# Kernel tuning notes

Measured on AMD Instinct MI355X. Metric: run time of the kernel, lower is better.

Reference implementation:

```python
import jax, jax.numpy as jnp
import numpy as np

B, T, D_IN = 64, 365, 10
D_MODEL, N_HEAD, D_K = 256, 16, 8
D_HEAD = D_MODEL // N_HEAD  # 16, value head dim
MAX_POS = 365 + 2 * 30      # max_position + 2*max_temporal_shift = 425
BN_EPS = 1e-5


def _pos_table(n_pos, d, temp=1000.0):
    # standard sinusoidal table (frozen in the original via Embedding.from_pretrained)
    pos = np.arange(n_pos)[:, None].astype(np.float64)
    i = np.arange(d)[None, :]
    angle = pos / np.power(temp, 2 * (i // 2) / d)
    tab = np.where(i % 2 == 0, np.sin(angle), np.cos(angle))
    return jnp.asarray(tab, jnp.float32)

POS_TABLE = _pos_table(MAX_POS, D_MODEL)


def _linear_layer(x, W, b, g, beta):
    # LinearLayer = Linear -> BatchNorm1d (train-mode batch stats, per-feature) -> ReLU
    y = x @ W.T + b
    ax = tuple(range(y.ndim - 1))
    mu = y.mean(ax, keepdims=True)
    var = y.var(ax, keepdims=True)  # biased var, matches torch BN
    y = (y - mu) * jax.lax.rsqrt(var + BN_EPS) * g + beta
    return jax.nn.relu(y)


def _forward(positions, x, w1, b1, g1, e1, w2, b2, g2, e2, w3, b3, g3, e3,
             ws1, ws2, wi, bi, gi, ei, wk, bk, wq, bq, wm, bm, gm, em,
             wd1, bd1, gd1, ed1, wd2, bd2, gd2, ed2, wc, bc):
    # channel MLP encoder: 10 -> 64 -> 128 -> 256
    out = _linear_layer(x, w1, b1, g1, e1)
    out = _linear_layer(out, w2, b2, g2, e2)
    out = _linear_layer(out, w3, b3, g3, e3)                    # [B,T,256]
    # channel SE attention: avgpool over time, 2 linears (no bias), sigmoid, residual
    pooled = out.mean(axis=1, keepdims=True)                     # [B,1,256]
    att = jax.nn.sigmoid(jax.nn.relu(pooled @ ws1.T) @ ws2.T)    # [B,1,256]
    out = att * pooled + out                                     # broadcast residual
    # temporal attention block
    h = _linear_layer(out, wi, bi, gi, ei)                       # inconv -> [B,T,256]
    e = h + POS_TABLE[positions]                                 # add positional encoding
    q = (e @ wq.T + bq).reshape(B, T, N_HEAD, D_K)
    k = (e @ wk.T + bk).reshape(B, T, N_HEAD, D_K)
    v = e.reshape(B, T, N_HEAD, D_HEAD)
    # 'cross' attention: full score matrix, mean over key dim, softmax over query dim
    scores = jnp.einsum('bthd,bshd->bhts', q, k) / jnp.sqrt(jnp.float32(D_K))  # [B,H,T,T]
    scores = scores.mean(axis=-1)                                # [B,H,T]
    a = jax.nn.softmax(scores, axis=-1)                          # [B,H,T]
    y = jnp.einsum('bht,bthe->bhe', a, v).reshape(B, D_MODEL)    # [B,256]
    y = _linear_layer(y, wm, bm, gm, em)                         # mlp 256 -> 128
    # decoder: 128 -> 64 -> 32 -> num_classes
    z = _linear_layer(y, wd1, bd1, gd1, ed1)
    z = _linear_layer(z, wd2, bd2, gd2, ed2)
    return z @ wc.T + bc                                         # logits [B,10]


def setup_inputs():
    key = jax.random.key(0)
    ks = jax.random.split(key, 16)
    n = lambda i, sh: jax.random.normal(ks[i], sh, jnp.float32) * 0.05
    z, o = jnp.zeros, jnp.ones
    return {
        'x': jax.random.normal(ks[0], (B, T, D_IN), jnp.float32),
        'positions': jnp.sort(jax.random.randint(ks[1], (B, T), 0, MAX_POS), axis=-1),
        'w1': n(2, (64, D_IN)), 'b1': z(64), 'g1': o(64), 'e1': z(64),
        'w2': n(3, (128, 64)), 'b2': z(128), 'g2': o(128), 'e2': z(128),
        'w3': n(4, (256, 128)), 'b3': z(256), 'g3': o(256), 'e3': z(256),
        'ws1': n(5, (16, 256)), 'ws2': n(6, (256, 16)),
        'wi': n(7, (256, 256)), 'bi': z(256), 'gi': o(256), 'ei': z(256),
        'wk': n(8, (128, 256)), 'bk': z(128),
        'wq': n(9, (128, 256)), 'bq': z(128),
        'wm': n(10, (128, 256)), 'bm': z(128), 'gm': o(128), 'em': z(128),
        'wd1': n(11, (64, 128)), 'bd1': z(64), 'gd1': o(64), 'ed1': z(64),
        'wd2': n(12, (32, 64)), 'bd2': z(32), 'gd2': o(32), 'ed2': z(32),
        'wc': n(13, (10, 32)), 'bc': z(10),
    }


def reference(x, positions, w1, b1, g1, e1, w2, b2, g2, e2, w3, b3, g3, e3,
              ws1, ws2, wi, bi, gi, ei, wk, bk, wq, bq, wm, bm, gm, em,
              wd1, bd1, gd1, ed1, wd2, bd2, gd2, ed2, wc, bc):
    return _forward(positions, x, w1, b1, g1, e1, w2, b2, g2, e2, w3, b3, g3, e3,
                    ws1, ws2, wi, bi, gi, ei, wk, bk, wq, bq, wm, bm, gm, em,
                    wd1, bd1, gd1, ed1, wd2, bd2, gd2, ed2, wc, bc)
```

## Files before the change

kernel.cpp:

```cpp
#include <hip/hip_runtime.h>
#include <hip/hip_bf16.h>
#include <math.h>

#define TT 365
#define BT 23360
#define NPOS 425

typedef __hip_bfloat16 bf16;
typedef __attribute__((ext_vector_type(8))) short s16x8;
typedef __attribute__((ext_vector_type(4))) float f32x4;

__device__ __forceinline__ float b2f(bf16 v) { return __bfloat162float(v); }
__device__ __forceinline__ bf16  f2b(float v) { return __float2bfloat16(v); }
__device__ __forceinline__ float u2f(unsigned u) { return __uint_as_float(u); }
__device__ __forceinline__ short f2bs(float v) { bf16 h = __float2bfloat16(v); return *reinterpret_cast<short*>(&h); }
__device__ __forceinline__ void unpack8(uint4 raw, float* v) {
    v[0] = u2f(raw.x << 16); v[1] = u2f(raw.x & 0xffff0000u);
    v[2] = u2f(raw.y << 16); v[3] = u2f(raw.y & 0xffff0000u);
    v[4] = u2f(raw.z << 16); v[5] = u2f(raw.z & 0xffff0000u);
    v[6] = u2f(raw.w << 16); v[7] = u2f(raw.w & 0xffff0000u);
}

__global__ __launch_bounds__(256) void prep_kernel(
    float* __restrict__ stats, float* __restrict__ pooled, float* __restrict__ esum,
    const float* __restrict__ w2, const float* __restrict__ w3, const float* __restrict__ wi,
    const float* __restrict__ wq,
    bf16* __restrict__ whi, bf16* __restrict__ wlo, float* __restrict__ tab)
{
    int i = blockIdx.x * 256 + threadIdx.x;
    if (i < 2048)  { stats[i] = 0.f; return; }  i -= 2048;
    if (i < 16384) { pooled[i] = 0.f; return; } i -= 16384;
    if (i < 16384) { esum[i] = 0.f; return; }   i -= 16384;
    if (i < 139264) {
        float w;
        if      (i < 8192)   w = w2[i];
        else if (i < 40960)  w = w3[i - 8192];
        else if (i < 106496) w = wi[i - 40960];
        else                 w = wq[i - 106496];
        bf16 h = f2b(w);
        whi[i] = h;
        wlo[i] = f2b(w - b2f(h));
        return;
    } i -= 139264;
    if (i < 108800) {
        int c = i & 255, p = i >> 8;
        float e = (float)(2 * (c >> 1)) * (1.f / 256.f);
        float ang = (float)p * exp2f(-e * 9.96578428466209f);
        tab[i] = (c & 1) ? cosf(ang) : sinf(ang);
    }
}

__global__ __launch_bounds__(256) void gemm_l1_kernel(
    const float* __restrict__ x,
    const float* __restrict__ W, const float* __restrict__ bias,
    bf16* __restrict__ Y, float* __restrict__ stats)
{
    const int t  = threadIdx.x;
    const int tx = t & 15, ty = t >> 4;
    const int row0 = blockIdx.x * 64;
    __shared__ float As[64][17];
    __shared__ float Ws[16][65];
    __shared__ float red_s[4][64];
    __shared__ float red_q[4][64];
    float acc[4][4];
#pragma unroll
    for (int rr = 0; rr < 4; ++rr)
#pragma unroll
        for (int cc = 0; cc < 4; ++cc) acc[rr][cc] = 0.f;
#pragma unroll
    for (int i = 0; i < 4; ++i) {
        int idx = t + i * 256, r = idx >> 4, c = idx & 15;
        As[r][c] = (c < 10) ? x[(size_t)(row0 + r) * 10 + c] : 0.f;
    }
#pragma unroll
    for (int i = 0; i < 4; ++i) {
        int idx = t + i * 256, c = idx >> 4, kk = idx & 15;
        Ws[kk][c] = (kk < 10) ? W[(size_t)c * 10 + kk] : 0.f;
    }
    __syncthreads();
#pragma unroll
    for (int kk = 0; kk < 10; ++kk) {
        float a[4];
#pragma unroll
        for (int rr = 0; rr < 4; ++rr) a[rr] = As[ty * 4 + rr][kk];
#pragma unroll
        for (int cc = 0; cc < 4; ++cc) {
            float w = Ws[kk][cc * 16 + tx];
#pragma unroll
            for (int rr = 0; rr < 4; ++rr) acc[rr][cc] = fmaf(a[rr], w, acc[rr][cc]);
        }
    }
    float s_cc[4], q_cc[4];
#pragma unroll
    for (int cc = 0; cc < 4; ++cc) { s_cc[cc] = 0.f; q_cc[cc] = 0.f; }
#pragma unroll
    for (int rr = 0; rr < 4; ++rr) {
        int row = row0 + ty * 4 + rr;
#pragma unroll
        for (int cc = 0; cc < 4; ++cc) {
            int col = cc * 16 + tx;
            float v = acc[rr][cc] + bias[col];
            Y[(size_t)row * 64 + col] = f2b(v);
            s_cc[cc] += v; q_cc[cc] += v * v;
        }
    }
    int w = t >> 6;
#pragma unroll
    for (int cc = 0; cc < 4; ++cc) {
        float s = s_cc[cc], q = q_cc[cc];
        s += __shfl_xor(s, 16); q += __shfl_xor(q, 16);
        s += __shfl_xor(s, 32); q += __shfl_xor(q, 32);
        if ((t & 63) < 16) { red_s[w][cc * 16 + tx] = s; red_q[w][cc * 16 + tx] = q; }
    }
    __syncthreads();
    if (t < 64) {
        float s = red_s[0][t] + red_s[1][t] + red_s[2][t] + red_s[3][t];
        float q = red_q[0][t] + red_q[1][t] + red_q[2][t] + red_q[3][t];
        atomicAdd(&stats[t], s);
        atomicAdd(&stats[256 + t], q);
    }
}

template<int MODE, int K>
__global__ __launch_bounds__(256) void mfma_gemm(
    const bf16* __restrict__ A,
    const bf16* __restrict__ Whi, const bf16* __restrict__ Wlo,
    const float* __restrict__ bias,
    bf16* __restrict__ Y, int ldY, float* __restrict__ stats,
    const float* __restrict__ bnstats, const float* __restrict__ bng,
    const float* __restrict__ bnb, const float* __restrict__ sebuf)
{
    constexpr int KC = (K > 128) ? 128 : K;
    __shared__ s16x8 Wl[2][KC / 8][64];
    __shared__ float red_s[4][64];
    __shared__ float red_q[4][64];
    __shared__ float scb[MODE ? K : 1];
    __shared__ float shb[MODE ? K : 1];
    const int t = threadIdx.x, wave = t >> 6, lane = t & 63;
    const int n16 = lane & 15, quad = lane >> 4;
    const int m0 = blockIdx.x * 64 + wave * 16;
    const int col0 = blockIdx.y * 64;
    const int sc_ = t & 63, skg0 = t >> 6;
    const bf16* gh = Whi + (size_t)(col0 + sc_) * K;
    const bf16* gl = Wlo + (size_t)(col0 + sc_) * K;
#pragma unroll
    for (int kg = skg0; kg < KC / 8; kg += 4) {
        Wl[0][kg][sc_] = *(const s16x8*)(gh + kg * 8);
        Wl[1][kg][sc_] = *(const s16x8*)(gl + kg * 8);
    }
    if (MODE) {
        if (t < K) {
            float mu = bnstats[t] * (1.f / (float)BT);
            float var = bnstats[256 + t] * (1.f / (float)BT) - mu * mu;
            float sc = rsqrtf(var + 1e-5f) * bng[t];
            scb[t] = sc; shb[t] = bnb[t] - mu * sc;
        }
    }
    __syncthreads();
    const int arow = m0 + n16;
    const float* sev = (MODE == 2) ? (sebuf + (arow / TT) * 256) : nullptr;
    const bf16* Ap = A + (size_t)arow * K + quad * 8;
    s16x8 af[K / 32];
#pragma unroll
    for (int i = 0; i < K / 32; ++i) {
        s16x8 raw = *(const s16x8*)(Ap + i * 32);
        if (MODE) {
            int kb = i * 32 + quad * 8;
#pragma unroll
            for (int j = 0; j < 8; ++j) {
                float y = u2f(((unsigned)(unsigned short)raw[j]) << 16);
                float v = fmaxf(fmaf(y, scb[kb + j], shb[kb + j]), 0.f);
                if (MODE == 2) v += sev[kb + j];
                raw[j] = f2bs(v);
            }
        }
        af[i] = raw;
    }
    f32x4 acc[4];
    f32x4 zero = {0.f, 0.f, 0.f, 0.f};
#pragma unroll
    for (int ct = 0; ct < 4; ++ct) acc[ct] = zero;
#pragma unroll
    for (int kc = 0; kc < K; kc += KC) {
        if (kc) {
            __syncthreads();
#pragma unroll
            for (int kg = skg0; kg < KC / 8; kg += 4) {
                Wl[0][kg][sc_] = *(const s16x8*)(gh + kc + kg * 8);
                Wl[1][kg][sc_] = *(const s16x8*)(gl + kc + kg * 8);
            }
            __syncthreads();
        }
#pragma unroll
        for (int i = 0; i < KC / 32; ++i) {
            const int kgq = i * 4 + quad;
            const s16x8 a = af[(kc >> 5) + i];
#pragma unroll
            for (int ct = 0; ct < 4; ++ct) {
                s16x8 bl = Wl[1][kgq][ct * 16 + n16];
                s16x8 bh = Wl[0][kgq][ct * 16 + n16];
                acc[ct] = __builtin_amdgcn_mfma_f32_16x16x32_bf16(a, bl, acc[ct], 0, 0, 0);
                acc[ct] = __builtin_amdgcn_mfma_f32_16x16x32_bf16(a, bh, acc[ct], 0, 0, 0);
            }
        }
    }
#pragma unroll
    for (int ct = 0; ct < 4; ++ct) {
        int col = col0 + ct * 16 + n16;
        float bv = bias[col];
        float s = 0.f, q = 0.f;
#pragma unroll
        for (int r = 0; r < 4; ++r) {
            float v = acc[ct][r] + bv;
            int row = m0 + quad * 4 + r;
            Y[(size_t)row * ldY + col] = f2b(v);
            s += v; q += v * v;
        }
        s += __shfl_xor(s, 16); q += __shfl_xor(q, 16);
        s += __shfl_xor(s, 32); q += __shfl_xor(q, 32);
        if (quad == 0) { red_s[wave][ct * 16 + n16] = s; red_q[wave][ct * 16 + n16] = q; }
    }
    if (stats) {
        __syncthreads();
        if (t < 64) {
            float s = red_s[0][t] + red_s[1][t] + red_s[2][t] + red_s[3][t];
            float q = red_q[0][t] + red_q[1][t] + red_q[2][t] + red_q[3][t];
            atomicAdd(&stats[col0 + t], s);
            atomicAdd(&stats[256 + col0 + t], q);
        }
    }
}

__global__ __launch_bounds__(256) void pool_partial_kernel(
    const bf16* __restrict__ Y3, const float* __restrict__ stats,
    const float* __restrict__ g3, const float* __restrict__ e3,
    float* __restrict__ pooled)
{
    const int b = blockIdx.x, part = blockIdx.y, t = threadIdx.x;
    const int cg = t & 31, rs = t >> 5;
    __shared__ float scb[256], shb[256];
    __shared__ float pp[8][256];
    {
        float mu = stats[t] * (1.f / (float)BT);
        float var = stats[256 + t] * (1.f / (float)BT) - mu * mu;
        float sc = rsqrtf(var + 1e-5f) * g3[t];
        scb[t] = sc; shb[t] = e3[t] - mu * sc;
    }
    __syncthreads();
    float acc[8] = {0.f,0.f,0.f,0.f,0.f,0.f,0.f,0.f};
    const int r0 = part * 46;
#pragma unroll
    for (int i = 0; i < 6; ++i) {
        int l = rs + i * 8;
        int r = r0 + l;
        if (l < 46 && r < TT) {
            uint4 raw = *(const uint4*)(Y3 + ((size_t)b * TT + r) * 256 + cg * 8);
            float v[8];
            unpack8(raw, v);
#pragma unroll
            for (int j = 0; j < 8; ++j)
                acc[j] += fmaxf(fmaf(v[j], scb[cg * 8 + j], shb[cg * 8 + j]), 0.f);
        }
    }
#pragma unroll
    for (int j = 0; j < 8; ++j) pp[rs][cg * 8 + j] = acc[j];
    __syncthreads();
    float s = 0.f;
#pragma unroll
    for (int r = 0; r < 8; ++r) s += pp[r][t];
    atomicAdd(&pooled[b * 256 + t], s);
}

__global__ __launch_bounds__(256) void esum_kernel(const bf16* __restrict__ e,
                                                   float* __restrict__ esum)
{
    const int b = blockIdx.x, part = blockIdx.y, t = threadIdx.x;
    const int cg = t & 31, rs = t >> 5;
    __shared__ float pp[8][256];
    float acc[8] = {0.f,0.f,0.f,0.f,0.f,0.f,0.f,0.f};
    const int r0 = part * 46;
#pragma unroll
    for (int i = 0; i < 6; ++i) {
        int l = rs + i * 8;
        int r = r0 + l;
        if (l < 46 && r < TT) {
            uint4 raw = *(const uint4*)(e + ((size_t)b * TT + r) * 256 + cg * 8);
            float v[8];
            unpack8(raw, v);
#pragma unroll
            for (int j = 0; j < 8; ++j) acc[j] += v[j];
        }
    }
#pragma unroll
    for (int j = 0; j < 8; ++j) pp[rs][cg * 8 + j] = acc[j];
    __syncthreads();
    float s = 0.f;
#pragma unroll
    for (int r = 0; r < 8; ++r) s += pp[r][t];
    atomicAdd(&esum[b * 256 + t], s);
}

__global__ __launch_bounds__(256) void se_mlp_kernel(const float* __restrict__ pooled,
                                                     const float* __restrict__ ws1,
                                                     const float* __restrict__ ws2,
                                                     float* __restrict__ se) {
    int b = blockIdx.x, f = threadIdx.x;
    __shared__ float pl[256];
    __shared__ float hidden[16];
    float p = pooled[b * 256 + f] * (1.f / (float)TT);
    pl[f] = p;
    __syncthreads();
    if (f < 16) {
        float h = 0.f;
        for (int k2 = 0; k2 < 256; ++k2) h = fmaf(pl[k2], ws1[f * 256 + k2], h);
        hidden[f] = fmaxf(h, 0.f);
    }
    __syncthreads();
    float a = 0.f;
    for (int k2 = 0; k2 < 16; ++k2) a = fmaf(hidden[k2], ws2[f * 16 + k2], a);
    a = 1.f / (1.f + expf(-a));
    se[b * 256 + f] = a * p;
}

__global__ __launch_bounds__(256) void bnrelu8_kernel(
    const bf16* __restrict__ Y, const float* __restrict__ stats,
    const float* __restrict__ g, const float* __restrict__ beta,
    bf16* __restrict__ Out, const float* __restrict__ tab, const int* __restrict__ pos) {
    int i = (blockIdx.x * 256 + threadIdx.x) * 8;
    int col = i & 255, row = i >> 8;
    uint4 raw = *(const uint4*)(Y + i);
    float v[8];
    unpack8(raw, v);
    const float invM = 1.f / (float)BT;
    const float* tr = tab + pos[row] * 256 + col;
    bf16 tmp[8] __attribute__((aligned(16)));
#pragma unroll
    for (int j = 0; j < 8; ++j) {
        float mu  = stats[col + j] * invM;
        float var = stats[256 + col + j] * invM - mu * mu;
        float o = (v[j] - mu) * rsqrtf(var + 1e-5f) * g[col + j] + beta[col + j];
        tmp[j] = f2b(fmaxf(o, 0.f) + tr[j]);
    }
    *(uint4*)(Out + i) = *(const uint4*)tmp;
}

__global__ __launch_bounds__(64) void attn_kernel(
    const bf16* __restrict__ q, const bf16* __restrict__ e,
    const float* __restrict__ esum, const float* __restrict__ wk,
    const float* __restrict__ bk, float* __restrict__ yv)
{
    __shared__ float aw[368];
    const int b = blockIdx.x, h = blockIdx.y;
    const int lane = threadIdx.x;
    float4 es = *(const float4*)(esum + b * 256 + lane * 4);
    float ks[8];
#pragma unroll
    for (int d = 0; d < 8; ++d) {
        float4 wv = *(const float4*)(wk + (size_t)(h * 8 + d) * 256 + lane * 4);
        ks[d] = es.x * wv.x + es.y * wv.y + es.z * wv.z + es.w * wv.w;
    }
#pragma unroll
    for (int off = 1; off < 64; off <<= 1)
#pragma unroll
        for (int d = 0; d < 8; ++d) ks[d] += __shfl_xor(ks[d], off);
#pragma unroll
    for (int d = 0; d < 8; ++d) ks[d] += (float)TT * bk[h * 8 + d];
    const float scale = 1.f / (sqrtf(8.f) * (float)TT);
    const bf16* qb = q + (size_t)b * TT * 128 + h * 8;
    float sv[6];
    float m = -1e30f;
#pragma unroll
    for (int i = 0; i < 6; ++i) {
        int r = lane + i * 64;
        float s = -1e30f;
        if (r < TT) {
            uint4 raw = *(const uint4*)(qb + (size_t)r * 128);
            float v[8];
            unpack8(raw, v);
            float dot = 0.f;
#pragma unroll
            for (int j = 0; j < 8; ++j) dot = fmaf(v[j], ks[j], dot);
            s = dot * scale;
        }
        sv[i] = s;
        m = fmaxf(m, s);
    }
#pragma unroll
    for (int off = 1; off < 64; off <<= 1) m = fmaxf(m, __shfl_xor(m, off));
    float sum = 0.f;
#pragma unroll
    for (int i = 0; i < 6; ++i) {
        float ev = (sv[i] > -1e29f) ? expf(sv[i] - m) : 0.f;
        sv[i] = ev; sum += ev;
    }
#pragma unroll
    for (int off = 1; off < 64; off <<= 1) sum += __shfl_xor(sum, off);
    float inv = 1.f / sum;
#pragma unroll
    for (int i = 0; i < 6; ++i) {
        int r = lane + i * 64;
        if (r < TT) aw[r] = sv[i] * inv;
    }
    __syncthreads();
    const int half = lane & 1, rs = lane >> 1;
    float acc[8] = {0.f,0.f,0.f,0.f,0.f,0.f,0.f,0.f};
    const bf16* ebase = e + (size_t)b * TT * 256 + h * 16 + half * 8;
#pragma unroll
    for (int i = 0; i < 12; ++i) {
        int r = rs + i * 32;
        if (r < TT) {
            uint4 raw = *(const uint4*)(ebase + (size_t)r * 256);
            float v[8];
            unpack8(raw, v);
            float a = aw[r];
#pragma unroll
            for (int j = 0; j < 8; ++j) acc[j] = fmaf(a, v[j], acc[j]);
        }
    }
#pragma unroll
    for (int off = 2; off < 64; off <<= 1)
#pragma unroll
        for (int j = 0; j < 8; ++j) acc[j] += __shfl_xor(acc[j], off);
    if (lane < 2) {
        float* op = yv + b * 256 + h * 16 + half * 8;
#pragma unroll
        for (int j = 0; j < 8; ++j) op[j] = acc[j];
    }
}


__global__ __launch_bounds__(256) void tail_m_kernel(
    const float* __restrict__ yv, const float* __restrict__ wm,
    const float* __restrict__ gm, const float* __restrict__ em,
    float* __restrict__ z1)
{
    __shared__ float Xq[4160];
    const int t = threadIdx.x, r = t & 63, cw = t >> 6;
    const int c0 = blockIdx.x * 8 + cw * 2;
    const float4* wf4 = (const float4*)wm;
    float acc[2] = {0.f, 0.f};
    for (int p = 0; p < 4; ++p) {
        if (p) __syncthreads();
        for (int i = t; i < 4096; i += 256) {
            int kk = i & 63, rr = i >> 6;
            Xq[kk * 65 + rr] = yv[rr * 256 + p * 64 + kk];
        }
        __syncthreads();
#pragma unroll 4
        for (int k4 = 0; k4 < 16; ++k4) {
            float xv[4];
#pragma unroll
            for (int j = 0; j < 4; ++j) xv[j] = Xq[(k4 * 4 + j) * 65 + r];
#pragma unroll
            for (int c = 0; c < 2; ++c) {
                float4 w = wf4[(c0 + c) * 64 + p * 16 + k4];
                acc[c] = fmaf(xv[0], w.x, acc[c]);
                acc[c] = fmaf(xv[1], w.y, acc[c]);
                acc[c] = fmaf(xv[2], w.z, acc[c]);
                acc[c] = fmaf(xv[3], w.w, acc[c]);
            }
        }
    }
#pragma unroll
    for (int c = 0; c < 2; ++c) {
        float v = acc[c];
        float s = v, q = v * v;
#pragma unroll
        for (int off = 1; off < 64; off <<= 1) { s += __shfl_xor(s, off); q += __shfl_xor(q, off); }
        float mu = s * (1.f / 64.f), var = q * (1.f / 64.f) - mu * mu;
        float sc = rsqrtf(var + 1e-5f) * gm[c0 + c], sh = em[c0 + c] - mu * sc;
        z1[r * 128 + c0 + c] = fmaxf(fmaf(v, sc, sh), 0.f);
    }
}

__global__ __launch_bounds__(256) void tail_d1_kernel(
    const float* __restrict__ z1, const float* __restrict__ wd1,
    const float* __restrict__ gd1, const float* __restrict__ ed1,
    float* __restrict__ z2)
{
    __shared__ float Xq[4160];
    const int t = threadIdx.x, r = t & 63, cw = t >> 6;
    const int c0 = blockIdx.x * 8 + cw * 2;
    const float4* wf4 = (const float4*)wd1;
    float acc[2] = {0.f, 0.f};
    for (int p = 0; p < 2; ++p) {
        if (p) __syncthreads();
        for (int i = t; i < 4096; i += 256) {
            int kk = i & 63, rr = i >> 6;
            Xq[kk * 65 + rr] = z1[rr * 128 + p * 64 + kk];
        }
        __syncthreads();
#pragma unroll 4
        for (int k4 = 0; k4 < 16; ++k4) {
            float xv[4];
#pragma unroll
            for (int j = 0; j < 4; ++j) xv[j] = Xq[(k4 * 4 + j) * 65 + r];
#pragma unroll
            for (int c = 0; c < 2; ++c) {
                float4 w = wf4[(c0 + c) * 32 + p * 16 + k4];
                acc[c] = fmaf(xv[0], w.x, acc[c]);
                acc[c] = fmaf(xv[1], w.y, acc[c]);
                acc[c] = fmaf(xv[2], w.z, acc[c]);
                acc[c] = fmaf(xv[3], w.w, acc[c]);
            }
        }
    }
#pragma unroll
    for (int c = 0; c < 2; ++c) {
        float v = acc[c];
        float s = v, q = v * v;
#pragma unroll
        for (int off = 1; off < 64; off <<= 1) { s += __shfl_xor(s, off); q += __shfl_xor(q, off); }
        float mu = s * (1.f / 64.f), var = q * (1.f / 64.f) - mu * mu;
        float sc = rsqrtf(var + 1e-5f) * gd1[c0 + c], sh = ed1[c0 + c] - mu * sc;
        z2[r * 64 + c0 + c] = fmaxf(fmaf(v, sc, sh), 0.f);
    }
}

__global__ __launch_bounds__(256) void tail_d2c_kernel(
    const float* __restrict__ z2, const float* __restrict__ wd2,
    const float* __restrict__ gd2, const float* __restrict__ ed2,
    const float* __restrict__ wc, const float* __restrict__ bc,
    float* __restrict__ out)
{
    __shared__ float Xq[4160];
    __shared__ float Z3t[2048];
    __shared__ float WcL[320];
    const int t = threadIdx.x, r = t & 63, cw = t >> 6;
    const int c03 = cw * 8;
    for (int i = t; i < 4096; i += 256) {
        int kk = i & 63, rr = i >> 6;
        Xq[kk * 65 + rr] = z2[rr * 64 + kk];
    }
    if (t < 80) ((float4*)WcL)[t] = ((const float4*)wc)[t];
    __syncthreads();
    const float4* wf4 = (const float4*)wd2;
    float acc[8] = {0.f,0.f,0.f,0.f,0.f,0.f,0.f,0.f};
#pragma unroll 4
    for (int k4 = 0; k4 < 16; ++k4) {
        float xv[4];
#pragma unroll
        for (int j = 0; j < 4; ++j) xv[j] = Xq[(k4 * 4 + j) * 65 + r];
#pragma unroll
        for (int c = 0; c < 8; ++c) {
            float4 w = wf4[(c03 + c) * 16 + k4];
            acc[c] = fmaf(xv[0], w.x, acc[c]);
            acc[c] = fmaf(xv[1], w.y, acc[c]);
            acc[c] = fmaf(xv[2], w.z, acc[c]);
            acc[c] = fmaf(xv[3], w.w, acc[c]);
        }
    }
#pragma unroll
    for (int c = 0; c < 8; ++c) {
        float v = acc[c];
        float s = v, q = v * v;
#pragma unroll
        for (int off = 1; off < 64; off <<= 1) { s += __shfl_xor(s, off); q += __shfl_xor(q, off); }
        float mu = s * (1.f / 64.f), var = q * (1.f / 64.f) - mu * mu;
        float sc = rsqrtf(var + 1e-5f) * gd2[c03 + c], sh = ed2[c03 + c] - mu * sc;
        Z3t[(c03 + c) * 64 + r] = fmaxf(fmaf(v, sc, sh), 0.f);
    }
    __syncthreads();
#pragma unroll
    for (int i = 0; i < 3; ++i) {
        int idx = t + i * 256;
        if (idx < 640) {
            int rr = idx / 10, c = idx - rr * 10;
            float s = bc[c];
#pragma unroll
            for (int kk = 0; kk < 32; ++kk) s = fmaf(Z3t[kk * 64 + rr], WcL[c * 32 + kk], s);
            out[idx] = s;
        }
    }
}


extern "C" void kernel_launch(void* const* d_in, const int* in_sizes, int n_in,
                              void* d_out, int out_size, void* d_ws, size_t ws_size,
                              hipStream_t stream) {
    (void)in_sizes; (void)n_in; (void)out_size; (void)ws_size;
    const float* x  = (const float*)d_in[0];
    const int* pos  = (const int*)d_in[1];
    const float *w1 = (const float*)d_in[2],  *b1 = (const float*)d_in[3],
                *g1 = (const float*)d_in[4],  *e1 = (const float*)d_in[5];
    const float *w2 = (const float*)d_in[6],  *b2 = (const float*)d_in[7],
                *g2 = (const float*)d_in[8],  *e2 = (const float*)d_in[9];
    const float *w3 = (const float*)d_in[10], *b3 = (const float*)d_in[11],
                *g3 = (const float*)d_in[12], *e3 = (const float*)d_in[13];
    const float *ws1 = (const float*)d_in[14], *ws2 = (const float*)d_in[15];
    const float *wi = (const float*)d_in[16], *bi = (const float*)d_in[17],
                *gi = (const float*)d_in[18], *ei = (const float*)d_in[19];
    const float *wk = (const float*)d_in[20], *bk = (const float*)d_in[21];
    const float *wq = (const float*)d_in[22], *bq = (const float*)d_in[23];
    const float *wm = (const float*)d_in[24], *bm = (const float*)d_in[25],
                *gm = (const float*)d_in[26], *em = (const float*)d_in[27];
    const float *wd1 = (const float*)d_in[28], *bd1 = (const float*)d_in[29],
                *gd1 = (const float*)d_in[30], *ed1 = (const float*)d_in[31];
    const float *wd2 = (const float*)d_in[32], *bd2 = (const float*)d_in[33],
                *gd2 = (const float*)d_in[34], *ed2 = (const float*)d_in[35];
    const float *wc = (const float*)d_in[36], *bc = (const float*)d_in[37];
    float* out = (float*)d_out;
    (void)bm; (void)bd1; (void)bd2;

    char* w8 = (char*)d_ws;
    bf16*  actA   = (bf16*)(w8);
    bf16*  actB   = (bf16*)(w8 + 11960320);
    bf16*  whi    = (bf16*)(w8 + 23920640);
    bf16*  wlo    = (bf16*)(w8 + 24199168);
    float* tab    = (float*)(w8 + 24477696);
    float* stats  = (float*)(w8 + 24912896);
    float* pooled = (float*)(w8 + 24921088);
    float* sebuf  = (float*)(w8 + 24986624);
    float* esum   = (float*)(w8 + 25052160);
    float* yvb    = (float*)(w8 + 25117696);
    float* z1     = esum;
    float* z2     = sebuf;

    prep_kernel<<<1105, 256, 0, stream>>>(stats, pooled, esum, w2, w3, wi, wq, whi, wlo, tab);
    gemm_l1_kernel<<<365, 256, 0, stream>>>(x, w1, b1, actB, stats);
    mfma_gemm<1, 64><<<dim3(365, 2), 256, 0, stream>>>(actB, whi, wlo, b2,
                                                       actA, 128, stats + 512, stats, g1, e1, nullptr);
    mfma_gemm<1, 128><<<dim3(365, 4), 256, 0, stream>>>(actA, whi + 8192, wlo + 8192, b3,
                                                        actB, 256, stats + 1024, stats + 512, g2, e2, nullptr);
    pool_partial_kernel<<<dim3(64, 8), 256, 0, stream>>>(actB, stats + 1024, g3, e3, pooled);
    se_mlp_kernel<<<64, 256, 0, stream>>>(pooled, ws1, ws2, sebuf);
    mfma_gemm<2, 256><<<dim3(365, 4), 256, 0, stream>>>(actB, whi + 40960, wlo + 40960, bi,
                                                        actA, 256, stats + 1536, stats + 1024, g3, e3, sebuf);
    bnrelu8_kernel<<<BT * 256 / 2048, 256, 0, stream>>>(actA, stats + 1536, gi, ei, actB, tab, pos);
    esum_kernel<<<dim3(64, 8), 256, 0, stream>>>(actB, esum);
    mfma_gemm<0, 256><<<dim3(365, 2), 256, 0, stream>>>(actB, whi + 106496, wlo + 106496, bq,
                                                        actA, 128, nullptr, nullptr, nullptr, nullptr, nullptr);
    attn_kernel<<<dim3(64, 16), 64, 0, stream>>>(actA, actB, esum, wk, bk, yvb);
    tail_m_kernel<<<16, 256, 0, stream>>>(yvb, wm, gm, em, z1);
    tail_d1_kernel<<<8, 256, 0, stream>>>(z1, wd1, gd1, ed1, z2);
    tail_d2c_kernel<<<1, 256, 0, stream>>>(z2, wd2, gd2, ed2, wc, bc, out);
}
```

Before: 316.0 us.

## Fuse key-sum reduction into per-batch attention kernel, drop esum launch

Removes the separate esum kernel and its atomics, computing the time-sum of e inside a new attention kernel with one 256-thread block per batch that handles all 16 heads. The block computes the summed key projection once in shared memory, scores all heads into a shared buffer, runs the softmax per head with one wave per four heads, then does the weighted value sum with one thread per output feature. This removes a launch and the redundant per-head key recomputation, but leaves only 64 blocks, which may underuse the GPU. Each block reads e twice with 2-byte scalar loads instead of vector loads.

```diff
diff --git a/kernel.cpp b/kernel.cpp
--- a/kernel.cpp
+++ b/kernel.cpp
@@ -271,35 +271,6 @@
     atomicAdd(&pooled[b * 256 + t], s);
 }
 
-__global__ __launch_bounds__(256) void esum_kernel(const bf16* __restrict__ e,
-                                                   float* __restrict__ esum)
-{
-    const int b = blockIdx.x, part = blockIdx.y, t = threadIdx.x;
-    const int cg = t & 31, rs = t >> 5;
-    __shared__ float pp[8][256];
-    float acc[8] = {0.f,0.f,0.f,0.f,0.f,0.f,0.f,0.f};
-    const int r0 = part * 46;
-#pragma unroll
-    for (int i = 0; i < 6; ++i) {
-        int l = rs + i * 8;
-        int r = r0 + l;
-        if (l < 46 && r < TT) {
-            uint4 raw = *(const uint4*)(e + ((size_t)b * TT + r) * 256 + cg * 8);
-            float v[8];
-            unpack8(raw, v);
-#pragma unroll
-            for (int j = 0; j < 8; ++j) acc[j] += v[j];
-        }
-    }
-#pragma unroll
-    for (int j = 0; j < 8; ++j) pp[rs][cg * 8 + j] = acc[j];
-    __syncthreads();
-    float s = 0.f;
-#pragma unroll
-    for (int r = 0; r < 8; ++r) s += pp[r][t];
-    atomicAdd(&esum[b * 256 + t], s);
-}
-
 __global__ __launch_bounds__(256) void se_mlp_kernel(const float* __restrict__ pooled,
                                                      const float* __restrict__ ws1,
                                                      const float* __restrict__ ws2,
@@ -344,87 +315,102 @@
     *(uint4*)(Out + i) = *(const uint4*)tmp;
 }
 
-__global__ __launch_bounds__(64) void attn_kernel(
+__global__ __launch_bounds__(256) void attn2_kernel(
     const bf16* __restrict__ q, const bf16* __restrict__ e,
-    const float* __restrict__ esum, const float* __restrict__ wk,
-    const float* __restrict__ bk, float* __restrict__ yv)
-{
-    __shared__ float aw[368];
-    const int b = blockIdx.x, h = blockIdx.y;
-    const int lane = threadIdx.x;
-    float4 es = *(const float4*)(esum + b * 256 + lane * 4);
-    float ks[8];
-#pragma unroll
-    for (int d = 0; d < 8; ++d) {
-        float4 wv = *(const float4*)(wk + (size_t)(h * 8 + d) * 256 + lane * 4);
-        ks[d] = es.x * wv.x + es.y * wv.y + es.z * wv.z + es.w * wv.w;
-    }
-#pragma unroll
-    for (int off = 1; off < 64; off <<= 1)
-#pragma unroll
-        for (int d = 0; d < 8; ++d) ks[d] += __shfl_xor(ks[d], off);
-#pragma unroll
-    for (int d = 0; d < 8; ++d) ks[d] += (float)TT * bk[h * 8 + d];
-    const float scale = 1.f / (sqrtf(8.f) * (float)TT);
-    const bf16* qb = q + (size_t)b * TT * 128 + h * 8;
-    float sv[6];
-    float m = -1e30f;
-#pragma unroll
-    for (int i = 0; i < 6; ++i) {
-        int r = lane + i * 64;
-        float s = -1e30f;
-        if (r < TT) {
-            uint4 raw = *(const uint4*)(qb + (size_t)r * 128);
-            float v[8];
-            unpack8(raw, v);
-            float dot = 0.f;
-#pragma unroll
-            for (int j = 0; j < 8; ++j) dot = fmaf(v[j], ks[j], dot);
-            s = dot * scale;
-        }
-        sv[i] = s;
-        m = fmaxf(m, s);
-    }
-#pragma unroll
-    for (int off = 1; off < 64; off <<= 1) m = fmaxf(m, __shfl_xor(m, off));
-    float sum = 0.f;
-#pragma unroll
-    for (int i = 0; i < 6; ++i) {
-        float ev = (sv[i] > -1e29f) ? expf(sv[i] - m) : 0.f;
-        sv[i] = ev; sum += ev;
-    }
-#pragma unroll
-    for (int off = 1; off < 64; off <<= 1) sum += __shfl_xor(sum, off);
-    float inv = 1.f / sum;
-#pragma unroll
-    for (int i = 0; i < 6; ++i) {
-        int r = lane + i * 64;
-        if (r < TT) aw[r] = sv[i] * inv;
-    }
-    __syncthreads();
-    const int half = lane & 1, rs = lane >> 1;
-    float acc[8] = {0.f,0.f,0.f,0.f,0.f,0.f,0.f,0.f};
-    const bf16* ebase = e + (size_t)b * TT * 256 + h * 16 + half * 8;
-#pragma unroll
-    for (int i = 0; i < 12; ++i) {
-        int r = rs + i * 32;
-        if (r < TT) {
-            uint4 raw = *(const uint4*)(ebase + (size_t)r * 256);
-            float v[8];
-            unpack8(raw, v);
-            float a = aw[r];
-#pragma unroll
-            for (int j = 0; j < 8; ++j) acc[j] = fmaf(a, v[j], acc[j]);
-        }
-    }
-#pragma unroll
-    for (int off = 2; off < 64; off <<= 1)
-#pragma unroll
-        for (int j = 0; j < 8; ++j) acc[j] += __shfl_xor(acc[j], off);
-    if (lane < 2) {
-        float* op = yv + b * 256 + h * 16 + half * 8;
-#pragma unroll
-        for (int j = 0; j < 8; ++j) op[j] = acc[j];
+    const float* __restrict__ wk, const float* __restrict__ bk,
+    float* __restrict__ yv)
+{
+    __shared__ float esL[256];
+    __shared__ float ksL[128];
+    __shared__ float aw[16 * 369];
+    const int b = blockIdx.x, t = threadIdx.x;
+    const int lane = t & 63, w = t >> 6;
+    const bf16* eb = e + (size_t)b * TT * 256 + t;
+    {
+        float acc[5] = {0.f, 0.f, 0.f, 0.f, 0.f};
+        for (int i = 0; i < 73; ++i) {
+#pragma unroll
+            for (int s = 0; s < 5; ++s)
+                acc[s] += b2f(eb[(size_t)(i + s * 73) * 256]);
+        }
+        esL[t] = acc[0] + acc[1] + acc[2] + acc[3] + acc[4];
+    }
+    __syncthreads();
+    if (t < 128) {
+        const float4* wk4 = (const float4*)(wk + (size_t)t * 256);
+        const float4* es4 = (const float4*)esL;
+        float dot = 0.f;
+#pragma unroll 8
+        for (int k4 = 0; k4 < 64; ++k4) {
+            float4 a = es4[k4];
+            float4 wv = wk4[k4];
+            dot += a.x * wv.x + a.y * wv.y + a.z * wv.z + a.w * wv.w;
+        }
+        ksL[t] = dot + (float)TT * bk[t];
+    }
+    __syncthreads();
+    {
+        const int h = t & 15, tg = t >> 4;
+        float kreg[8];
+#pragma unroll
+        for (int d = 0; d < 8; ++d) kreg[d] = ksL[h * 8 + d];
+        const float scale = 1.f / (sqrtf(8.f) * (float)TT);
+        const bf16* qb = q + (size_t)b * TT * 128 + h * 8;
+#pragma unroll
+        for (int i = 0; i < 23; ++i) {
+            int r = tg + i * 16;
+            if (r < TT) {
+                uint4 raw = *(const uint4*)(qb + (size_t)r * 128);
+                float v[8];
+                unpack8(raw, v);
+                float dot = 0.f;
+#pragma unroll
+                for (int j = 0; j < 8; ++j) dot = fmaf(v[j], kreg[j], dot);
+                aw[h * 369 + r] = dot * scale;
+            }
+        }
+    }
+    __syncthreads();
+#pragma unroll
+    for (int j = 0; j < 4; ++j) {
+        const int h = w * 4 + j;
+        float sv[6];
+        float m = -1e30f;
+#pragma unroll
+        for (int i = 0; i < 6; ++i) {
+            int r = lane + i * 64;
+            sv[i] = (r < TT) ? aw[h * 369 + r] : -1e30f;
+            m = fmaxf(m, sv[i]);
+        }
+#pragma unroll
+        for (int off = 1; off < 64; off <<= 1) m = fmaxf(m, __shfl_xor(m, off));
+        float sum = 0.f;
+#pragma unroll
+        for (int i = 0; i < 6; ++i) {
+            float ev = (sv[i] > -1e29f) ? expf(sv[i] - m) : 0.f;
+            sv[i] = ev; sum += ev;
+        }
+#pragma unroll
+        for (int off = 1; off < 64; off <<= 1) sum += __shfl_xor(sum, off);
+        float inv = 1.f / sum;
+#pragma unroll
+        for (int i = 0; i < 6; ++i) {
+            int r = lane + i * 64;
+            if (r < TT) aw[h * 369 + r] = sv[i] * inv;
+        }
+    }
+    __syncthreads();
+    {
+        const int hb = (t >> 4) * 369;
+        float acc[5] = {0.f, 0.f, 0.f, 0.f, 0.f};
+        for (int i = 0; i < 73; ++i) {
+#pragma unroll
+            for (int s = 0; s < 5; ++s) {
+                int r = i + s * 73;
+                acc[s] = fmaf(aw[hb + r], b2f(eb[(size_t)r * 256]), acc[s]);
+            }
+        }
+        yv[b * 256 + t] = acc[0] + acc[1] + acc[2] + acc[3] + acc[4];
     }
 }
 
@@ -627,10 +613,9 @@
     mfma_gemm<2, 256><<<dim3(365, 4), 256, 0, stream>>>(actB, whi + 40960, wlo + 40960, bi,
                                                         actA, 256, stats + 1536, stats + 1024, g3, e3, sebuf);
     bnrelu8_kernel<<<BT * 256 / 2048, 256, 0, stream>>>(actA, stats + 1536, gi, ei, actB, tab, pos);
-    esum_kernel<<<dim3(64, 8), 256, 0, stream>>>(actB, esum);
     mfma_gemm<0, 256><<<dim3(365, 2), 256, 0, stream>>>(actB, whi + 106496, wlo + 106496, bq,
                                                         actA, 128, nullptr, nullptr, nullptr, nullptr, nullptr);
-    attn_kernel<<<dim3(64, 16), 64, 0, stream>>>(actA, actB, esum, wk, bk, yvb);
+    attn2_kernel<<<64, 256, 0, stream>>>(actA, actB, wk, bk, yvb);
     tail_m_kernel<<<16, 256, 0, stream>>>(yvb, wm, gm, em, z1);
     tail_d1_kernel<<<8, 256, 0, stream>>>(z1, wd1, gd1, ed1, z2);
     tail_d2c_kernel<<<1, 256, 0, stream>>>(z2, wd2, gd2, ed2, wc, bc, out);
```

Result: slower. 339.8 us (+7.6%).

## Fold query projection into per-head key vector and fuse esum into bnrelu

Applied to the files above, without the earlier changes.

The per-(batch, head) attention score, q·ksum, is rewritten as e·(Wq^T ksum) + bq·ksum. This removes the separate Q projection GEMM and its intermediate buffer, and the attention kernel now reads the 256-wide e rows directly. The esum reduction is also fused into the bnrelu kernel through a shared-memory partial sum and atomics, which removes one full pass over e. In exchange, the attention kernel reads 256 bf16 values per row instead of 8 and adds atomic contention in bnrelu.

```diff
diff --git a/kernel.cpp b/kernel.cpp
--- a/kernel.cpp
+++ b/kernel.cpp
@@ -271,35 +271,6 @@
     atomicAdd(&pooled[b * 256 + t], s);
 }
 
-__global__ __launch_bounds__(256) void esum_kernel(const bf16* __restrict__ e,
-                                                   float* __restrict__ esum)
-{
-    const int b = blockIdx.x, part = blockIdx.y, t = threadIdx.x;
-    const int cg = t & 31, rs = t >> 5;
-    __shared__ float pp[8][256];
-    float acc[8] = {0.f,0.f,0.f,0.f,0.f,0.f,0.f,0.f};
-    const int r0 = part * 46;
-#pragma unroll
-    for (int i = 0; i < 6; ++i) {
-        int l = rs + i * 8;
-        int r = r0 + l;
-        if (l < 46 && r < TT) {
-            uint4 raw = *(const uint4*)(e + ((size_t)b * TT + r) * 256 + cg * 8);
-            float v[8];
-            unpack8(raw, v);
-#pragma unroll
-            for (int j = 0; j < 8; ++j) acc[j] += v[j];
-        }
-    }
-#pragma unroll
-    for (int j = 0; j < 8; ++j) pp[rs][cg * 8 + j] = acc[j];
-    __syncthreads();
-    float s = 0.f;
-#pragma unroll
-    for (int r = 0; r < 8; ++r) s += pp[r][t];
-    atomicAdd(&esum[b * 256 + t], s);
-}
-
 __global__ __launch_bounds__(256) void se_mlp_kernel(const float* __restrict__ pooled,
                                                      const float* __restrict__ ws1,
                                                      const float* __restrict__ ws2,
@@ -325,8 +296,11 @@
 __global__ __launch_bounds__(256) void bnrelu8_kernel(
     const bf16* __restrict__ Y, const float* __restrict__ stats,
     const float* __restrict__ g, const float* __restrict__ beta,
-    bf16* __restrict__ Out, const float* __restrict__ tab, const int* __restrict__ pos) {
-    int i = (blockIdx.x * 256 + threadIdx.x) * 8;
+    bf16* __restrict__ Out, const float* __restrict__ tab, const int* __restrict__ pos,
+    float* __restrict__ esum) {
+    __shared__ float pe[8][256];
+    const int t = threadIdx.x;
+    int i = (blockIdx.x * 256 + t) * 8;
     int col = i & 255, row = i >> 8;
     uint4 raw = *(const uint4*)(Y + i);
     float v[8];
@@ -334,21 +308,38 @@
     const float invM = 1.f / (float)BT;
     const float* tr = tab + pos[row] * 256 + col;
     bf16 tmp[8] __attribute__((aligned(16)));
+    float* pr = &pe[t >> 5][col];
 #pragma unroll
     for (int j = 0; j < 8; ++j) {
         float mu  = stats[col + j] * invM;
         float var = stats[256 + col + j] * invM - mu * mu;
         float o = (v[j] - mu) * rsqrtf(var + 1e-5f) * g[col + j] + beta[col + j];
-        tmp[j] = f2b(fmaxf(o, 0.f) + tr[j]);
+        float ev = fmaxf(o, 0.f) + tr[j];
+        tmp[j] = f2b(ev);
+        pr[j] = ev;
     }
     *(uint4*)(Out + i) = *(const uint4*)tmp;
-}
-
-__global__ __launch_bounds__(64) void attn_kernel(
-    const bf16* __restrict__ q, const bf16* __restrict__ e,
-    const float* __restrict__ esum, const float* __restrict__ wk,
-    const float* __restrict__ bk, float* __restrict__ yv)
-{
+    __syncthreads();
+    const int g0 = blockIdx.x * 8;
+    const int b0 = g0 / TT, b1 = (g0 + 7) / TT;
+    const int split = (b1 != b0) ? (b1 * TT - g0) : 8;
+    float s0 = 0.f, s1 = 0.f;
+#pragma unroll
+    for (int rr = 0; rr < 8; ++rr) {
+        float vv = pe[rr][t];
+        if (rr < split) s0 += vv; else s1 += vv;
+    }
+    atomicAdd(&esum[b0 * 256 + t], s0);
+    if (b1 != b0) atomicAdd(&esum[b1 * 256 + t], s1);
+}
+
+__global__ __launch_bounds__(64) void attn3_kernel(
+    const bf16* __restrict__ e, const float* __restrict__ esum,
+    const float* __restrict__ wk, const float* __restrict__ bk,
+    const float* __restrict__ wq, const float* __restrict__ bq,
+    float* __restrict__ yv)
+{
+    __shared__ float kqL[256];
     __shared__ float aw[368];
     const int b = blockIdx.x, h = blockIdx.y;
     const int lane = threadIdx.x;
@@ -365,25 +356,59 @@
         for (int d = 0; d < 8; ++d) ks[d] += __shfl_xor(ks[d], off);
 #pragma unroll
     for (int d = 0; d < 8; ++d) ks[d] += (float)TT * bk[h * 8 + d];
+    {
+        float4 kq = {0.f, 0.f, 0.f, 0.f};
+#pragma unroll
+        for (int d = 0; d < 8; ++d) {
+            float4 wv = *(const float4*)(wq + (size_t)(h * 8 + d) * 256 + lane * 4);
+            kq.x = fmaf(ks[d], wv.x, kq.x);
+            kq.y = fmaf(ks[d], wv.y, kq.y);
+            kq.z = fmaf(ks[d], wv.z, kq.z);
+            kq.w = fmaf(ks[d], wv.w, kq.w);
+        }
+        *(float4*)&kqL[lane * 4] = kq;
+    }
+    float cb = 0.f;
+#pragma unroll
+    for (int d = 0; d < 8; ++d) cb = fmaf(ks[d], bq[h * 8 + d], cb);
+    __syncthreads();
+    const int gp = lane >> 3, gl = lane & 7;
+    float4 kr[8];
+    {
+        const float4* kq4 = (const float4*)(kqL + gl * 32);
+#pragma unroll
+        for (int u = 0; u < 8; ++u) kr[u] = kq4[u];
+    }
     const float scale = 1.f / (sqrtf(8.f) * (float)TT);
-    const bf16* qb = q + (size_t)b * TT * 128 + h * 8;
+    const bf16* ebs = e + (size_t)b * TT * 256 + gl * 32;
+    for (int it = 0; it < 46; ++it) {
+        int r = it * 8 + gp;
+        if (r < TT) {
+            const bf16* ep = ebs + (size_t)r * 256;
+            float dot = 0.f;
+#pragma unroll
+            for (int u = 0; u < 4; ++u) {
+                uint4 raw = *(const uint4*)(ep + u * 8);
+                float v[8];
+                unpack8(raw, v);
+                float4 ka = kr[u * 2], kb2 = kr[u * 2 + 1];
+                dot += v[0] * ka.x + v[1] * ka.y + v[2] * ka.z + v[3] * ka.w
+                     + v[4] * kb2.x + v[5] * kb2.y + v[6] * kb2.z + v[7] * kb2.w;
+            }
+            dot += __shfl_xor(dot, 1);
+            dot += __shfl_xor(dot, 2);
+            dot += __shfl_xor(dot, 4);
+            if (gl == 0) aw[r] = (dot + cb) * scale;
+        }
+    }
+    __syncthreads();
     float sv[6];
     float m = -1e30f;
 #pragma unroll
     for (int i = 0; i < 6; ++i) {
         int r = lane + i * 64;
-        float s = -1e30f;
-        if (r < TT) {
-            uint4 raw = *(const uint4*)(qb + (size_t)r * 128);
-            float v[8];
-            unpack8(raw, v);
-            float dot = 0.f;
-#pragma unroll
-            for (int j = 0; j < 8; ++j) dot = fmaf(v[j], ks[j], dot);
-            s = dot * scale;
-        }
-        sv[i] = s;
-        m = fmaxf(m, s);
+        sv[i] = (r < TT) ? aw[r] : -1e30f;
+        m = fmaxf(m, sv[i]);
     }
 #pragma unroll
     for (int off = 1; off < 64; off <<= 1) m = fmaxf(m, __shfl_xor(m, off));
@@ -626,11 +651,8 @@
     se_mlp_kernel<<<64, 256, 0, stream>>>(pooled, ws1, ws2, sebuf);
     mfma_gemm<2, 256><<<dim3(365, 4), 256, 0, stream>>>(actB, whi + 40960, wlo + 40960, bi,
                                                         actA, 256, stats + 1536, stats + 1024, g3, e3, sebuf);
-    bnrelu8_kernel<<<BT * 256 / 2048, 256, 0, stream>>>(actA, stats + 1536, gi, ei, actB, tab, pos);
-    esum_kernel<<<dim3(64, 8), 256, 0, stream>>>(actB, esum);
-    mfma_gemm<0, 256><<<dim3(365, 2), 256, 0, stream>>>(actB, whi + 106496, wlo + 106496, bq,
-                                                        actA, 128, nullptr, nullptr, nullptr, nullptr, nullptr);
-    attn_kernel<<<dim3(64, 16), 64, 0, stream>>>(actA, actB, esum, wk, bk, yvb);
+    bnrelu8_kernel<<<BT * 256 / 2048, 256, 0, stream>>>(actA, stats + 1536, gi, ei, actB, tab, pos, esum);
+    attn3_kernel<<<dim3(64, 16), 64, 0, stream>>>(actB, esum, wk, bk, wq, bq, yvb);
     tail_m_kernel<<<16, 256, 0, stream>>>(yvb, wm, gm, em, z1);
     tail_d1_kernel<<<8, 256, 0, stream>>>(z1, wd1, gd1, ed1, z2);
     tail_d2c_kernel<<<1, 256, 0, stream>>>(z2, wd2, gd2, ed2, wc, bc, out);
```

Measured after the change: 316.9 us. Within noise of the previous version (+0.3%).
